# Performance work log

Hardware: AMD Instinct MI355X
Metric: run time of the kernel (lower is better)

The kernel has to match this reference:

```python
import jax, jax.numpy as jnp
import numpy as np

N = 20000
E = 320000
IN_DIM = 128
HID = 64
HEADS = 8
OUT_DIM = 128
NEG_SLOPE = 0.2  # PyG GATConv default leaky_relu slope


def _glorot(key, shape):
    fan_in = shape[0] if len(shape) > 1 else shape[-1]
    return jax.random.normal(key, shape, dtype=jnp.float32) / jnp.sqrt(jnp.float32(fan_in))


def setup_inputs() -> dict:
    key = jax.random.key(0)
    ks = jax.random.split(key, 16)
    x = jax.random.normal(ks[0], (N, IN_DIM), dtype=jnp.float32)
    edge_index = jax.random.randint(ks[1], (2, E), 0, N, dtype=jnp.int32)
    HC = HEADS * HID
    return {
        "x": x,
        "edge_index": edge_index,
        # layer 1: in -> heads*hid (concat)
        "W1": _glorot(ks[2], (IN_DIM, HC)),
        "a_src1": _glorot(ks[3], (HEADS, HID)),
        "a_dst1": _glorot(ks[4], (HEADS, HID)),
        "b1": jnp.zeros((HC,), jnp.float32),
        # layer 2: heads*hid -> heads*hid (concat)
        "W2": _glorot(ks[5], (HC, HC)),
        "a_src2": _glorot(ks[6], (HEADS, HID)),
        "a_dst2": _glorot(ks[7], (HEADS, HID)),
        "b2": jnp.zeros((HC,), jnp.float32),
        # layer 3: heads*hid -> out, heads=1, concat=False
        "W3": _glorot(ks[8], (HC, OUT_DIM)),
        "a_src3": _glorot(ks[9], (1, OUT_DIM)),
        "a_dst3": _glorot(ks[10], (1, OUT_DIM)),
        "b3": jnp.zeros((OUT_DIM,), jnp.float32),
    }


def _gat_layer(x, src, dst, W, a_src, a_dst, b, heads, concat):
    # x: [N, F_in] -> h: [N, H, C]
    n = x.shape[0]
    h = (x @ W).reshape(n, heads, -1)
    # per-node attention half-logits: [N, H]
    al_src = jnp.sum(h * a_src[None], axis=-1)
    al_dst = jnp.sum(h * a_dst[None], axis=-1)
    # per-edge logits with leaky relu: [E, H]
    e = jax.nn.leaky_relu(al_src[src] + al_dst[dst], NEG_SLOPE)
    # segment softmax over incoming edges of each dst node
    emax = jax.ops.segment_max(e, dst, num_segments=n)
    ex = jnp.exp(e - emax[dst])
    den = jax.ops.segment_sum(ex, dst, num_segments=n)
    alpha = ex / (den[dst] + 1e-16)
    # weighted scatter-aggregate of source features: [E, H, C] -> [N, H, C]
    out = jax.ops.segment_sum(h[src] * alpha[:, :, None], dst, num_segments=n)
    out = out.reshape(n, -1) if concat else out.mean(axis=1)
    return out + b


def reference(x, edge_index, W1, a_src1, a_dst1, b1, W2, a_src2, a_dst2, b2,
              W3, a_src3, a_dst3, b3):
    # PyG GATConv adds self-loops by default
    loops = jnp.arange(N, dtype=edge_index.dtype)
    src = jnp.concatenate([edge_index[0], loops])
    dst = jnp.concatenate([edge_index[1], loops])
    # eval mode: dropout is identity
    h = _gat_layer(x, src, dst, W1, a_src1, a_dst1, b1, HEADS, True)
    h = jax.nn.elu(h)
    h = _gat_layer(h, src, dst, W2, a_src2, a_dst2, b2, HEADS, True)
    h = jax.nn.elu(h)
    out = _gat_layer(h, src, dst, W3, a_src3, a_dst3, b3, 1, False)
    return out
```

## Files before the change

### kernel.cpp

```cpp
#include <hip/hip_runtime.h>
#include <math.h>

#define NN 20000
#define EE 320000
#define ETOT 340000
#define NHEADS 8
#define HID 64
#define HCV 512
#define IND 128
#define OUTD 128
#define NEG_SLOPE 0.2f

typedef __attribute__((ext_vector_type(8))) _Float16 half8;
typedef __attribute__((ext_vector_type(4))) float floatx4;

__device__ __forceinline__ void cvt_one(const float* W, _Float16* T, int idx, int K, int N) {
    int k = idx / N, n = idx - k * N;
    T[(size_t)n * K + k] = (_Float16)W[idx];
}

#define S1 (IND * HCV)
#define S2 (HCV * HCV)
#define S3 (HCV * OUTD)
#define STOT (S1 + S2 + S3)
#define XTOT (NN * IND)
__global__ void prep_kernel(const float* __restrict__ W1, const float* __restrict__ W2,
                            const float* __restrict__ W3, const float* __restrict__ x,
                            _Float16* __restrict__ T1, _Float16* __restrict__ T2,
                            _Float16* __restrict__ T3, _Float16* __restrict__ xh,
                            int* __restrict__ cnt) {
    int idx = blockIdx.x * blockDim.x + threadIdx.x;
    if (idx < S1) cvt_one(W1, T1, idx, IND, HCV);
    else if (idx < S1 + S2) cvt_one(W2, T2, idx - S1, HCV, HCV);
    else if (idx < STOT) cvt_one(W3, T3, idx - S1 - S2, HCV, OUTD);
    else if (idx < STOT + NN) cnt[idx - STOT] = 0;
    else if (idx < STOT + NN + XTOT) {
        int j = idx - STOT - NN;
        xh[j] = (_Float16)x[j];
    }
}


__global__ void count_kernel(const int* __restrict__ ei, int* __restrict__ cnt) {
    int i = blockIdx.x * blockDim.x + threadIdx.x;
    if (i >= ETOT) return;
    int v = (i < EE) ? ei[EE + i] : (i - EE);
    atomicAdd(&cnt[v], 1);
}

#define SCH 20
__global__ __launch_bounds__(1024) void scan_kernel(const int* __restrict__ cnt,
                                                    int* __restrict__ row_ptr,
                                                    int* __restrict__ cursor) {
    __shared__ int wtot[16];
    __shared__ int woff[16];
    int t = threadIdx.x;
    int lane = t & 63;
    int wid = t >> 6;
    int base = t * SCH;
    int vals[SCH];
    int s = 0;
    #pragma unroll
    for (int i = 0; i < SCH; i++) {
        int idx = base + i;
        int v = (idx < NN) ? cnt[idx] : 0;
        vals[i] = v;
        s += v;
    }
    int incl = s;
    #pragma unroll
    for (int off = 1; off < 64; off <<= 1) {
        int u = __shfl_up(incl, off);
        if (lane >= off) incl += u;
    }
    int excl = incl - s;
    if (lane == 63) wtot[wid] = incl;
    __syncthreads();
    if (t == 0) {
        int run = 0;
        #pragma unroll
        for (int j = 0; j < 16; j++) { woff[j] = run; run += wtot[j]; }
        row_ptr[NN] = run;
    }
    __syncthreads();
    int run = woff[wid] + excl;
    #pragma unroll
    for (int i = 0; i < SCH; i++) {
        int idx = base + i;
        if (idx < NN) { row_ptr[idx] = run; cursor[idx] = run; run += vals[i]; }
    }
}

__global__ void fill_kernel(const int* __restrict__ ei, int* __restrict__ cursor,
                            int* __restrict__ csr_src) {
    int i = blockIdx.x * blockDim.x + threadIdx.x;
    if (i >= ETOT) return;
    int u, v;
    if (i < EE) { u = ei[i]; v = ei[EE + i]; }
    else        { u = i - EE; v = i - EE; }
    int pos = atomicAdd(&cursor[v], 1);
    csr_src[pos] = u;
}

#define LDK 40
__global__ __launch_bounds__(256) void gemm_al(const _Float16* __restrict__ A,
                                               const _Float16* __restrict__ Bt,
                                               _Float16* __restrict__ C16,
                                               const float* __restrict__ a_src,
                                               const float* __restrict__ a_dst,
                                               float* __restrict__ als2,
                                               float* __restrict__ ald2,
                                               int M, int K) {
    __shared__ _Float16 sA[64 * LDK];
    __shared__ _Float16 sB[128 * LDK];
    __shared__ float psum_s[4][64];
    __shared__ float psum_d[4][64];
    int tid = threadIdx.x;
    int lane = tid & 63;
    int wv = tid >> 6;
    int m0 = blockIdx.x * 64, n0 = blockIdx.y * 128;
    int quad = lane >> 4;
    int l15 = lane & 15;
    int arow = tid >> 2;
    int ac4 = tid & 3;

    floatx4 acc[4][2] = {};

    for (int k0 = 0; k0 < K; k0 += 32) {
        {
            int gm = m0 + arow;
            int4 va;
            if (gm < M) va = *(const int4*)&A[(size_t)gm * K + k0 + ac4 * 8];
            else        va = make_int4(0, 0, 0, 0);
            *(int4*)&sA[arow * LDK + ac4 * 8] = va;
            #pragma unroll
            for (int r = 0; r < 2; r++) {
                int gn = n0 + arow + r * 64;
                int4 vb = *(const int4*)&Bt[(size_t)gn * K + k0 + ac4 * 8];
                *(int4*)&sB[(arow + r * 64) * LDK + ac4 * 8] = vb;
            }
        }
        __syncthreads();
        half8 a[4], b[2];
        #pragma unroll
        for (int i = 0; i < 4; i++)
            a[i] = *(const half8*)&sA[(i * 16 + l15) * LDK + quad * 8];
        #pragma unroll
        for (int j = 0; j < 2; j++)
            b[j] = *(const half8*)&sB[(wv * 32 + j * 16 + l15) * LDK + quad * 8];
        #pragma unroll
        for (int i = 0; i < 4; i++)
            #pragma unroll
            for (int j = 0; j < 2; j++)
                acc[i][j] = __builtin_amdgcn_mfma_f32_16x16x32_f16(a[i], b[j], acc[i][j], 0, 0, 0);
        __syncthreads();
    }
    #pragma unroll
    for (int i = 0; i < 4; i++) {
        #pragma unroll
        for (int r = 0; r < 4; r++) {
            int gm = m0 + i * 16 + quad * 4 + r;
            if (gm < M) {
                #pragma unroll
                for (int j = 0; j < 2; j++)
                    C16[(size_t)gm * HCV + n0 + wv * 32 + j * 16 + l15] = (_Float16)acc[i][j][r];
            }
        }
    }
    int h0 = n0 >> 6;
    float as_v[2], ad_v[2];
    #pragma unroll
    for (int j = 0; j < 2; j++) {
        int dim = (wv * 32 + j * 16 + l15) & 63;
        int hh = h0 + (wv >> 1);
        as_v[j] = a_src[hh * HID + dim];
        ad_v[j] = a_dst[hh * HID + dim];
    }
    #pragma unroll
    for (int i = 0; i < 4; i++) {
        #pragma unroll
        for (int r = 0; r < 4; r++) {
            float ps = acc[i][0][r] * as_v[0] + acc[i][1][r] * as_v[1];
            float pd = acc[i][0][r] * ad_v[0] + acc[i][1][r] * ad_v[1];
            #pragma unroll
            for (int off = 1; off <= 8; off <<= 1) {
                ps += __shfl_xor(ps, off);
                pd += __shfl_xor(pd, off);
            }
            if (l15 == 0) {
                int row = i * 16 + quad * 4 + r;
                psum_s[wv][row] = ps;
                psum_d[wv][row] = pd;
            }
        }
    }
    __syncthreads();
    if (tid < 64) {
        int gm = m0 + tid;
        if (gm < M) {
            als2[(size_t)h0 * NN + gm]       = psum_s[0][tid] + psum_s[1][tid];
            als2[(size_t)(h0 + 1) * NN + gm] = psum_s[2][tid] + psum_s[3][tid];
            ald2[(size_t)h0 * NN + gm]       = psum_d[0][tid] + psum_d[1][tid];
            ald2[(size_t)(h0 + 1) * NN + gm] = psum_d[2][tid] + psum_d[3][tid];
        }
    }
}

__global__ __launch_bounds__(256) void gemm3(const _Float16* __restrict__ A,
                                             const _Float16* __restrict__ Bt,
                                             _Float16* __restrict__ C16,
                                             const float* __restrict__ a_src,
                                             const float* __restrict__ a_dst,
                                             float* __restrict__ als,
                                             float* __restrict__ ald,
                                             int M, int K) {
    __shared__ _Float16 sA[64 * LDK];
    __shared__ _Float16 sB[128 * LDK];
    __shared__ float psum_s[4][64];
    __shared__ float psum_d[4][64];
    int tid = threadIdx.x;
    int lane = tid & 63;
    int wv = tid >> 6;
    int m0 = blockIdx.x * 64;
    int quad = lane >> 4;
    int l15 = lane & 15;
    int arow = tid >> 2;
    int ac4 = tid & 3;

    floatx4 acc[4][2] = {};

    for (int k0 = 0; k0 < K; k0 += 32) {
        {
            int gm = m0 + arow;
            int4 va;
            if (gm < M) va = *(const int4*)&A[(size_t)gm * K + k0 + ac4 * 8];
            else        va = make_int4(0, 0, 0, 0);
            *(int4*)&sA[arow * LDK + ac4 * 8] = va;
            #pragma unroll
            for (int r = 0; r < 2; r++) {
                int gn = arow + r * 64;
                int4 vb = *(const int4*)&Bt[(size_t)gn * K + k0 + ac4 * 8];
                *(int4*)&sB[(arow + r * 64) * LDK + ac4 * 8] = vb;
            }
        }
        __syncthreads();
        half8 a[4], b[2];
        #pragma unroll
        for (int i = 0; i < 4; i++)
            a[i] = *(const half8*)&sA[(i * 16 + l15) * LDK + quad * 8];
        #pragma unroll
        for (int j = 0; j < 2; j++)
            b[j] = *(const half8*)&sB[(wv * 32 + j * 16 + l15) * LDK + quad * 8];
        #pragma unroll
        for (int i = 0; i < 4; i++)
            #pragma unroll
            for (int j = 0; j < 2; j++)
                acc[i][j] = __builtin_amdgcn_mfma_f32_16x16x32_f16(a[i], b[j], acc[i][j], 0, 0, 0);
        __syncthreads();
    }
    #pragma unroll
    for (int i = 0; i < 4; i++) {
        #pragma unroll
        for (int r = 0; r < 4; r++) {
            int gm = m0 + i * 16 + quad * 4 + r;
            if (gm < M) {
                #pragma unroll
                for (int j = 0; j < 2; j++)
                    C16[(size_t)gm * OUTD + wv * 32 + j * 16 + l15] = (_Float16)acc[i][j][r];
            }
        }
    }
    float as_v[2], ad_v[2];
    #pragma unroll
    for (int j = 0; j < 2; j++) {
        as_v[j] = a_src[wv * 32 + j * 16 + l15];
        ad_v[j] = a_dst[wv * 32 + j * 16 + l15];
    }
    #pragma unroll
    for (int i = 0; i < 4; i++) {
        #pragma unroll
        for (int r = 0; r < 4; r++) {
            float ps = acc[i][0][r] * as_v[0] + acc[i][1][r] * as_v[1];
            float pd = acc[i][0][r] * ad_v[0] + acc[i][1][r] * ad_v[1];
            #pragma unroll
            for (int off = 1; off <= 8; off <<= 1) {
                ps += __shfl_xor(ps, off);
                pd += __shfl_xor(pd, off);
            }
            if (l15 == 0) {
                int row = i * 16 + quad * 4 + r;
                psum_s[wv][row] = ps;
                psum_d[wv][row] = pd;
            }
        }
    }
    __syncthreads();
    if (tid < 64) {
        int gm = m0 + tid;
        if (gm < M) {
            als[gm] = psum_s[0][tid] + psum_s[1][tid] + psum_s[2][tid] + psum_s[3][tid];
            ald[gm] = psum_d[0][tid] + psum_d[1][tid] + psum_d[2][tid] + psum_d[3][tid];
        }
    }
}

__global__ __launch_bounds__(256) void gather_kernel(const _Float16* __restrict__ h,
                                                     const int* __restrict__ row_ptr,
                                                     const int* __restrict__ csr_src,
                                                     const float* __restrict__ als2,
                                                     const float* __restrict__ ald2,
                                                     const float* __restrict__ bias,
                                                     _Float16* __restrict__ gout) {
    int tid = threadIdx.x;
    int lane = tid & 63;
    int wid = tid >> 6;
    int bid = blockIdx.x;
    int hd = bid & 7;
    int sub = lane >> 3;
    int dl = lane & 7;
    int v = (bid >> 3) * 32 + wid * 8 + sub;
    if (v >= NN) return;
    const float* asl = als2 + (size_t)hd * NN;
    float adst = ald2[(size_t)hd * NN + v];
    int s0 = row_ptr[v], s1 = row_ptr[v + 1];
    const _Float16* hh = h + hd * HID + dl * 8;
    float acc[8] = {};
    float l = 0.f;
    int j = s0;
    for (; j + 4 <= s1; j += 4) {
        int u[4]; float p[4]; half8 xv[4];
        #pragma unroll
        for (int e = 0; e < 4; e++) u[e] = csr_src[j + e];
        #pragma unroll
        for (int e = 0; e < 4; e++) xv[e] = *(const half8*)&hh[(size_t)u[e] * HCV];
        #pragma unroll
        for (int e = 0; e < 4; e++) {
            float t = asl[u[e]] + adst;
            t = (t > 0.f) ? t : NEG_SLOPE * t;
            p[e] = __expf(fminf(t, 80.f));
        }
        #pragma unroll
        for (int e = 0; e < 4; e++) {
            l += p[e];
            #pragma unroll
            for (int k = 0; k < 8; k++)
                acc[k] = fmaf(p[e], (float)xv[e][k], acc[k]);
        }
    }
    for (; j < s1; j++) {
        int u0 = csr_src[j];
        half8 x0 = *(const half8*)&hh[(size_t)u0 * HCV];
        float t0 = asl[u0] + adst;
        t0 = (t0 > 0.f) ? t0 : NEG_SLOPE * t0;
        float p0 = __expf(fminf(t0, 80.f));
        l += p0;
        #pragma unroll
        for (int k = 0; k < 8; k++)
            acc[k] = fmaf(p0, (float)x0[k], acc[k]);
    }
    float inv = 1.f / (l + 1e-16f);
    half8 hv;
    #pragma unroll
    for (int k = 0; k < 8; k++) {
        float o = fmaf(acc[k], inv, bias[hd * HID + dl * 8 + k]);
        o = (o > 0.f) ? o : (__expf(o) - 1.f);
        hv[k] = (_Float16)o;
    }
    half8* dst = (half8*)&gout[(size_t)v * HCV + hd * HID + dl * 8];
    __builtin_nontemporal_store(hv, dst);
}

__global__ __launch_bounds__(256) void gather3_kernel(const _Float16* __restrict__ h,
                                                      const int* __restrict__ row_ptr,
                                                      const int* __restrict__ csr_src,
                                                      const float* __restrict__ als,
                                                      const float* __restrict__ ald,
                                                      const float* __restrict__ bias,
                                                      float* __restrict__ out) {
    int lane = threadIdx.x & 63;
    int v = blockIdx.x * 4 + (threadIdx.x >> 6);
    if (v >= NN) return;
    int e_sub = lane >> 4;
    int cg = lane & 15;
    float adst = ald[v];
    int s0 = row_ptr[v], s1 = row_ptr[v + 1];
    float m = -INFINITY;
    for (int i = s0 + e_sub; i < s1; i += 4) {
        int u = csr_src[i];
        float t = als[u] + adst;
        t = (t > 0.f) ? t : NEG_SLOPE * t;
        m = fmaxf(m, t);
    }
    m = fmaxf(m, __shfl_xor(m, 16));
    m = fmaxf(m, __shfl_xor(m, 32));
    float acc[8] = {};
    float l = 0.f;
    for (int i = s0 + e_sub; i < s1; i += 4) {
        int u = csr_src[i];
        float t = als[u] + adst;
        t = (t > 0.f) ? t : NEG_SLOPE * t;
        float p = __expf(t - m);
        half8 x = *(const half8*)&h[(size_t)u * OUTD + cg * 8];
        l += p;
        #pragma unroll
        for (int j = 0; j < 8; j++)
            acc[j] = fmaf(p, (float)x[j], acc[j]);
    }
    l += __shfl_xor(l, 16);
    l += __shfl_xor(l, 32);
    #pragma unroll
    for (int j = 0; j < 8; j++) {
        acc[j] += __shfl_xor(acc[j], 16);
        acc[j] += __shfl_xor(acc[j], 32);
    }
    if (e_sub == 0) {
        float inv = 1.f / (l + 1e-16f);
        float4 o0, o1;
        o0.x = fmaf(acc[0], inv, bias[cg * 8 + 0]);
        o0.y = fmaf(acc[1], inv, bias[cg * 8 + 1]);
        o0.z = fmaf(acc[2], inv, bias[cg * 8 + 2]);
        o0.w = fmaf(acc[3], inv, bias[cg * 8 + 3]);
        o1.x = fmaf(acc[4], inv, bias[cg * 8 + 4]);
        o1.y = fmaf(acc[5], inv, bias[cg * 8 + 5]);
        o1.z = fmaf(acc[6], inv, bias[cg * 8 + 6]);
        o1.w = fmaf(acc[7], inv, bias[cg * 8 + 7]);
        *(float4*)&out[(size_t)v * OUTD + cg * 8] = o0;
        *(float4*)&out[(size_t)v * OUTD + cg * 8 + 4] = o1;
    }
}


extern "C" void kernel_launch(void* const* d_in, const int* in_sizes, int n_in,
                              void* d_out, int out_size, void* d_ws, size_t ws_size,
                              hipStream_t stream) {
    const float* x     = (const float*)d_in[0];
    const int*   ei    = (const int*)d_in[1];
    const float* W1    = (const float*)d_in[2];
    const float* as1   = (const float*)d_in[3];
    const float* ad1   = (const float*)d_in[4];
    const float* b1    = (const float*)d_in[5];
    const float* W2    = (const float*)d_in[6];
    const float* as2   = (const float*)d_in[7];
    const float* ad2   = (const float*)d_in[8];
    const float* b2    = (const float*)d_in[9];
    const float* W3    = (const float*)d_in[10];
    const float* as3   = (const float*)d_in[11];
    const float* ad3   = (const float*)d_in[12];
    const float* b3    = (const float*)d_in[13];
    float* out = (float*)d_out;

    size_t off = 0;
    auto carve = [&](size_t bytes) {
        void* p = (char*)d_ws + off;
        off += (bytes + 255) & ~(size_t)255;
        return p;
    };
    int* row_ptr   = (int*)carve((NN + 1) * sizeof(int));
    int* cursor    = (int*)carve(NN * sizeof(int));
    int* csr_src   = (int*)carve(ETOT * sizeof(int));
    _Float16* xh   = (_Float16*)carve((size_t)NN * IND * sizeof(_Float16));
    _Float16* h1   = (_Float16*)carve((size_t)NN * HCV * sizeof(_Float16));
    _Float16* gact = (_Float16*)carve((size_t)NN * HCV * sizeof(_Float16));
    _Float16* hf16 = (_Float16*)carve((size_t)NN * HCV * sizeof(_Float16));
    _Float16* h3   = (_Float16*)carve((size_t)NN * OUTD * sizeof(_Float16));
    float* als     = (float*)carve((size_t)NN * NHEADS * sizeof(float));
    float* ald     = (float*)carve((size_t)NN * NHEADS * sizeof(float));
    _Float16* W1T  = (_Float16*)carve((size_t)S1 * sizeof(_Float16));
    _Float16* W2T  = (_Float16*)carve((size_t)S2 * sizeof(_Float16));
    _Float16* W3T  = (_Float16*)carve((size_t)S3 * sizeof(_Float16));
    _Float16* gact2 = h1;
    (void)ws_size; (void)n_in; (void)in_sizes; (void)out_size;

    dim3 blk(256);

    int prep_n = STOT + NN + XTOT;
    prep_kernel<<<(prep_n + 255) / 256, blk, 0, stream>>>(W1, W2, W3, x,
        W1T, W2T, W3T, xh, cursor);

    count_kernel<<<(ETOT + 255) / 256, blk, 0, stream>>>(ei, cursor);
    scan_kernel<<<1, 1024, 0, stream>>>(cursor, row_ptr, cursor);
    fill_kernel<<<(ETOT + 255) / 256, blk, 0, stream>>>(ei, cursor, csr_src);

    int mt64 = (NN + 63) / 64;
    int nwaves_n = (NN + 3) / 4;
    int nb = (NN + 31) / 32;

    gemm_al<<<dim3(mt64, HCV / 128), blk, 0, stream>>>(xh, W1T, h1, as1, ad1, als, ald, NN, IND);
    gather_kernel<<<dim3(nb * 8), blk, 0, stream>>>(h1, row_ptr, csr_src, als, ald, b1, gact);

    gemm_al<<<dim3(mt64, HCV / 128), blk, 0, stream>>>(gact, W2T, hf16, as2, ad2, als, ald, NN, HCV);
    gather_kernel<<<dim3(nb * 8), blk, 0, stream>>>(hf16, row_ptr, csr_src, als, ald, b2, gact2);

    gemm3<<<dim3(mt64, 1), blk, 0, stream>>>(gact2, W3T, h3, as3, ad3, als, ald, NN, HCV);
    gather3_kernel<<<nwaves_n, blk, 0, stream>>>(h3, row_ptr, csr_src, als, ald, b3, out);
}
```

Measured before the change: 314.4 us.

## Use 128x128 GEMM tiles with 512 threads and remap layer-3 gather lanes

The attention GEMM now computes 128x128 output tiles with eight waves arranged 2x4, instead of 64x128 tiles with four waves. This halves the number of B-tile reloads per output row and the grid size, at the cost of more shared memory and fewer blocks. The final-layer gather is also restructured: eight lanes cover 64 columns of one node, each block covers half the feature width, and each lane walks the node's edges serially with a 2-way unroll. This removes the cross-subgroup shuffle reductions and puts more nodes in each wave. A harmless arow<64 guard is also added to gemm3's A load.

New measurement: 312.5 us. No clear change (-0.6%).

```diff
diff --git a/kernel.cpp b/kernel.cpp
--- a/kernel.cpp
+++ b/kernel.cpp
@@ -103,7 +103,7 @@
 }
 
 #define LDK 40
-__global__ __launch_bounds__(256) void gemm_al(const _Float16* __restrict__ A,
+__global__ __launch_bounds__(512) void gemm_al(const _Float16* __restrict__ A,
                                                const _Float16* __restrict__ Bt,
                                                _Float16* __restrict__ C16,
                                                const float* __restrict__ a_src,
@@ -111,14 +111,16 @@
                                                float* __restrict__ als2,
                                                float* __restrict__ ald2,
                                                int M, int K) {
-    __shared__ _Float16 sA[64 * LDK];
+    __shared__ _Float16 sA[128 * LDK];
     __shared__ _Float16 sB[128 * LDK];
-    __shared__ float psum_s[4][64];
-    __shared__ float psum_d[4][64];
+    __shared__ float psum_s[4][128];
+    __shared__ float psum_d[4][128];
     int tid = threadIdx.x;
     int lane = tid & 63;
-    int wv = tid >> 6;
-    int m0 = blockIdx.x * 64, n0 = blockIdx.y * 128;
+    int wid = tid >> 6;
+    int wv_m = wid >> 2;
+    int wv_n = wid & 3;
+    int m0 = blockIdx.x * 128, n0 = blockIdx.y * 128;
     int quad = lane >> 4;
     int l15 = lane & 15;
     int arow = tid >> 2;
@@ -133,21 +135,18 @@
             if (gm < M) va = *(const int4*)&A[(size_t)gm * K + k0 + ac4 * 8];
             else        va = make_int4(0, 0, 0, 0);
             *(int4*)&sA[arow * LDK + ac4 * 8] = va;
-            #pragma unroll
-            for (int r = 0; r < 2; r++) {
-                int gn = n0 + arow + r * 64;
-                int4 vb = *(const int4*)&Bt[(size_t)gn * K + k0 + ac4 * 8];
-                *(int4*)&sB[(arow + r * 64) * LDK + ac4 * 8] = vb;
-            }
+            int gn = n0 + arow;
+            int4 vb = *(const int4*)&Bt[(size_t)gn * K + k0 + ac4 * 8];
+            *(int4*)&sB[arow * LDK + ac4 * 8] = vb;
         }
         __syncthreads();
         half8 a[4], b[2];
         #pragma unroll
         for (int i = 0; i < 4; i++)
-            a[i] = *(const half8*)&sA[(i * 16 + l15) * LDK + quad * 8];
+            a[i] = *(const half8*)&sA[(wv_m * 64 + i * 16 + l15) * LDK + quad * 8];
         #pragma unroll
         for (int j = 0; j < 2; j++)
-            b[j] = *(const half8*)&sB[(wv * 32 + j * 16 + l15) * LDK + quad * 8];
+            b[j] = *(const half8*)&sB[(wv_n * 32 + j * 16 + l15) * LDK + quad * 8];
         #pragma unroll
         for (int i = 0; i < 4; i++)
             #pragma unroll
@@ -159,20 +158,20 @@
     for (int i = 0; i < 4; i++) {
         #pragma unroll
         for (int r = 0; r < 4; r++) {
-            int gm = m0 + i * 16 + quad * 4 + r;
+            int gm = m0 + wv_m * 64 + i * 16 + quad * 4 + r;
             if (gm < M) {
                 #pragma unroll
                 for (int j = 0; j < 2; j++)
-                    C16[(size_t)gm * HCV + n0 + wv * 32 + j * 16 + l15] = (_Float16)acc[i][j][r];
+                    C16[(size_t)gm * HCV + n0 + wv_n * 32 + j * 16 + l15] = (_Float16)acc[i][j][r];
             }
         }
     }
     int h0 = n0 >> 6;
+    int hh = h0 + (wv_n >> 1);
     float as_v[2], ad_v[2];
     #pragma unroll
     for (int j = 0; j < 2; j++) {
-        int dim = (wv * 32 + j * 16 + l15) & 63;
-        int hh = h0 + (wv >> 1);
+        int dim = (wv_n * 32 + j * 16 + l15) & 63;
         as_v[j] = a_src[hh * HID + dim];
         ad_v[j] = a_dst[hh * HID + dim];
     }
@@ -188,14 +187,14 @@
                 pd += __shfl_xor(pd, off);
             }
             if (l15 == 0) {
-                int row = i * 16 + quad * 4 + r;
-                psum_s[wv][row] = ps;
-                psum_d[wv][row] = pd;
+                int row = wv_m * 64 + i * 16 + quad * 4 + r;
+                psum_s[wv_n][row] = ps;
+                psum_d[wv_n][row] = pd;
             }
         }
     }
     __syncthreads();
-    if (tid < 64) {
+    if (tid < 128) {
         int gm = m0 + tid;
         if (gm < M) {
             als2[(size_t)h0 * NN + gm]       = psum_s[0][tid] + psum_s[1][tid];
@@ -233,9 +232,9 @@
         {
             int gm = m0 + arow;
             int4 va;
-            if (gm < M) va = *(const int4*)&A[(size_t)gm * K + k0 + ac4 * 8];
-            else        va = make_int4(0, 0, 0, 0);
-            *(int4*)&sA[arow * LDK + ac4 * 8] = va;
+            if (gm < M && arow < 64) va = *(const int4*)&A[(size_t)gm * K + k0 + ac4 * 8];
+            else                     va = make_int4(0, 0, 0, 0);
+            if (arow < 64) *(int4*)&sA[arow * LDK + ac4 * 8] = va;
             #pragma unroll
             for (int r = 0; r < 2; r++) {
                 int gn = arow + r * 64;
@@ -377,56 +376,69 @@
                                                       const float* __restrict__ ald,
                                                       const float* __restrict__ bias,
                                                       float* __restrict__ out) {
-    int lane = threadIdx.x & 63;
-    int v = blockIdx.x * 4 + (threadIdx.x >> 6);
+    int tid = threadIdx.x;
+    int lane = tid & 63;
+    int wid = tid >> 6;
+    int bid = blockIdx.x;
+    int dh = bid & 1;
+    int sub = lane >> 3;
+    int dl = lane & 7;
+    int v = (bid >> 1) * 32 + wid * 8 + sub;
     if (v >= NN) return;
-    int e_sub = lane >> 4;
-    int cg = lane & 15;
     float adst = ald[v];
     int s0 = row_ptr[v], s1 = row_ptr[v + 1];
+    const _Float16* hh = h + dh * 64 + dl * 8;
     float m = -INFINITY;
-    for (int i = s0 + e_sub; i < s1; i += 4) {
-        int u = csr_src[i];
+    for (int j = s0; j < s1; j++) {
+        int u = csr_src[j];
         float t = als[u] + adst;
         t = (t > 0.f) ? t : NEG_SLOPE * t;
         m = fmaxf(m, t);
     }
-    m = fmaxf(m, __shfl_xor(m, 16));
-    m = fmaxf(m, __shfl_xor(m, 32));
     float acc[8] = {};
     float l = 0.f;
-    for (int i = s0 + e_sub; i < s1; i += 4) {
-        int u = csr_src[i];
-        float t = als[u] + adst;
-        t = (t > 0.f) ? t : NEG_SLOPE * t;
-        float p = __expf(t - m);
-        half8 x = *(const half8*)&h[(size_t)u * OUTD + cg * 8];
-        l += p;
-        #pragma unroll
-        for (int j = 0; j < 8; j++)
-            acc[j] = fmaf(p, (float)x[j], acc[j]);
-    }
-    l += __shfl_xor(l, 16);
-    l += __shfl_xor(l, 32);
-    #pragma unroll
-    for (int j = 0; j < 8; j++) {
-        acc[j] += __shfl_xor(acc[j], 16);
-        acc[j] += __shfl_xor(acc[j], 32);
-    }
-    if (e_sub == 0) {
-        float inv = 1.f / (l + 1e-16f);
-        float4 o0, o1;
-        o0.x = fmaf(acc[0], inv, bias[cg * 8 + 0]);
-        o0.y = fmaf(acc[1], inv, bias[cg * 8 + 1]);
-        o0.z = fmaf(acc[2], inv, bias[cg * 8 + 2]);
-        o0.w = fmaf(acc[3], inv, bias[cg * 8 + 3]);
-        o1.x = fmaf(acc[4], inv, bias[cg * 8 + 4]);
-        o1.y = fmaf(acc[5], inv, bias[cg * 8 + 5]);
-        o1.z = fmaf(acc[6], inv, bias[cg * 8 + 6]);
-        o1.w = fmaf(acc[7], inv, bias[cg * 8 + 7]);
-        *(float4*)&out[(size_t)v * OUTD + cg * 8] = o0;
-        *(float4*)&out[(size_t)v * OUTD + cg * 8 + 4] = o1;
-    }
+    int j = s0;
+    for (; j + 2 <= s1; j += 2) {
+        int u0 = csr_src[j], u1 = csr_src[j + 1];
+        float t0 = als[u0] + adst;
+        float t1 = als[u1] + adst;
+        t0 = (t0 > 0.f) ? t0 : NEG_SLOPE * t0;
+        t1 = (t1 > 0.f) ? t1 : NEG_SLOPE * t1;
+        float p0 = __expf(t0 - m);
+        float p1 = __expf(t1 - m);
+        half8 x0 = *(const half8*)&hh[(size_t)u0 * OUTD];
+        half8 x1 = *(const half8*)&hh[(size_t)u1 * OUTD];
+        l += p0 + p1;
+        #pragma unroll
+        for (int k = 0; k < 8; k++) {
+            acc[k] = fmaf(p0, (float)x0[k], acc[k]);
+            acc[k] = fmaf(p1, (float)x1[k], acc[k]);
+        }
+    }
+    if (j < s1) {
+        int u0 = csr_src[j];
+        float t0 = als[u0] + adst;
+        t0 = (t0 > 0.f) ? t0 : NEG_SLOPE * t0;
+        float p0 = __expf(t0 - m);
+        half8 x0 = *(const half8*)&hh[(size_t)u0 * OUTD];
+        l += p0;
+        #pragma unroll
+        for (int k = 0; k < 8; k++)
+            acc[k] = fmaf(p0, (float)x0[k], acc[k]);
+    }
+    float inv = 1.f / (l + 1e-16f);
+    float4 o0, o1;
+    o0.x = fmaf(acc[0], inv, bias[dh * 64 + dl * 8 + 0]);
+    o0.y = fmaf(acc[1], inv, bias[dh * 64 + dl * 8 + 1]);
+    o0.z = fmaf(acc[2], inv, bias[dh * 64 + dl * 8 + 2]);
+    o0.w = fmaf(acc[3], inv, bias[dh * 64 + dl * 8 + 3]);
+    o1.x = fmaf(acc[4], inv, bias[dh * 64 + dl * 8 + 4]);
+    o1.y = fmaf(acc[5], inv, bias[dh * 64 + dl * 8 + 5]);
+    o1.z = fmaf(acc[6], inv, bias[dh * 64 + dl * 8 + 6]);
+    o1.w = fmaf(acc[7], inv, bias[dh * 64 + dl * 8 + 7]);
+    size_t base = (size_t)v * OUTD + dh * 64 + dl * 8;
+    *(float4*)&out[base] = o0;
+    *(float4*)&out[base + 4] = o1;
 }
 
 
@@ -482,15 +494,15 @@
     fill_kernel<<<(ETOT + 255) / 256, blk, 0, stream>>>(ei, cursor, csr_src);
 
     int mt64 = (NN + 63) / 64;
-    int nwaves_n = (NN + 3) / 4;
+    int mt128 = (NN + 127) / 128;
     int nb = (NN + 31) / 32;
 
-    gemm_al<<<dim3(mt64, HCV / 128), blk, 0, stream>>>(xh, W1T, h1, as1, ad1, als, ald, NN, IND);
+    gemm_al<<<dim3(mt128, HCV / 128), dim3(512), 0, stream>>>(xh, W1T, h1, as1, ad1, als, ald, NN, IND);
     gather_kernel<<<dim3(nb * 8), blk, 0, stream>>>(h1, row_ptr, csr_src, als, ald, b1, gact);
 
-    gemm_al<<<dim3(mt64, HCV / 128), blk, 0, stream>>>(gact, W2T, hf16, as2, ad2, als, ald, NN, HCV);
+    gemm_al<<<dim3(mt128, HCV / 128), dim3(512), 0, stream>>>(gact, W2T, hf16, as2, ad2, als, ald, NN, HCV);
     gather_kernel<<<dim3(nb * 8), blk, 0, stream>>>(hf16, row_ptr, csr_src, als, ald, b2, gact2);
 
     gemm3<<<dim3(mt64, 1), blk, 0, stream>>>(gact2, W3T, h3, as3, ad3, als, ald, NN, HCV);
-    gather3_kernel<<<nwaves_n, blk, 0, stream>>>(h3, row_ptr, csr_src, als, ald, b3, out);
-}
+    gather3_kernel<<<dim3(nb * 2), blk, 0, stream>>>(h3, row_ptr, csr_src, als, ald, b3, out);
+}
```
